# Kernel optimization log

Hardware: AMD Instinct MI355X
Metric: run time of the kernel (lower is better)

The kernel has to match this reference:

```python
import jax, jax.numpy as jnp
import numpy as np

DIM = 1024
HEADS = 16
HEAD_DIM = DIM // HEADS  # 64
EPS = 1e-5


def layer_norm(x, w, b):
    # LayerNorm over last dim (head_dim), matching nn.LayerNorm defaults
    mu = jnp.mean(x, axis=-1, keepdims=True)
    var = jnp.mean(jnp.square(x - mu), axis=-1, keepdims=True)
    return (x - mu) * jax.lax.rsqrt(var + EPS) * w + b


def apply_rotary_emb(x, freqs):
    # x: [B, S, H, D]; freqs: [S, D/2] angles. Interleaved (complex) rotary:
    # pairs (x[2i], x[2i+1]) rotated by angle freqs[:, i].
    x1 = x[..., 0::2]
    x2 = x[..., 1::2]
    cos = jnp.cos(freqs)[None, :, None, :]
    sin = jnp.sin(freqs)[None, :, None, :]
    r1 = x1 * cos - x2 * sin
    r2 = x1 * sin + x2 * cos
    return jnp.stack([r1, r2], axis=-1).reshape(x.shape)


def setup_inputs() -> dict:
    key = jax.random.key(0)
    ks = jax.random.split(key, 8)
    B, S = 2, 2048
    x = jax.random.normal(ks[0], (B, S, DIM), dtype=jnp.float32)
    freqs = jax.random.uniform(ks[1], (S, HEAD_DIM // 2), dtype=jnp.float32)
    sc = 1.0 / np.sqrt(DIM)
    w_qkv = jax.random.normal(ks[2], (DIM, 4 * DIM), dtype=jnp.float32) * sc
    w_out = jax.random.normal(ks[3], (DIM, DIM), dtype=jnp.float32) * sc
    qn_w = jnp.ones((HEAD_DIM,), jnp.float32)
    qn_b = jnp.zeros((HEAD_DIM,), jnp.float32)
    kn_w = jnp.ones((HEAD_DIM,), jnp.float32)
    kn_b = jnp.zeros((HEAD_DIM,), jnp.float32)
    return {"x": x, "freqs": freqs, "w_qkv": w_qkv, "w_out": w_out,
            "qn_w": qn_w, "qn_b": qn_b, "kn_w": kn_w, "kn_b": kn_b}


def reference(x, freqs, w_qkv, w_out, qn_w, qn_b, kn_w, kn_b):
    B, S, _ = x.shape
    qkv = x @ w_qkv  # [B, S, 4*DIM]
    q, k, v, gate = jnp.split(qkv, 4, axis=-1)
    q = q.reshape(B, S, HEADS, HEAD_DIM)
    k = k.reshape(B, S, HEADS, HEAD_DIM)
    v = v.reshape(B, S, HEADS, HEAD_DIM)
    q = layer_norm(q, qn_w, qn_b)
    k = layer_norm(k, kn_w, kn_b)
    q = apply_rotary_emb(q, freqs)
    k = apply_rotary_emb(k, freqs)
    # flash_attn_func: non-causal softmax attention, scale 1/sqrt(head_dim)
    scale = 1.0 / np.sqrt(HEAD_DIM)
    scores = jnp.einsum('bqhd,bkhd->bhqk', q, k) * scale
    probs = jax.nn.softmax(scores, axis=-1)
    o = jnp.einsum('bhqk,bkhd->bqhd', probs, v)
    o = o.reshape(B, S, DIM)
    o = o * jax.nn.sigmoid(gate)
    return o @ w_out
```

## Files before the change

kernel.cpp:

```cpp
#include <hip/hip_runtime.h>


typedef _Float16 f16;
typedef _Float16 f16x8 __attribute__((ext_vector_type(8)));
typedef _Float16 f16x4 __attribute__((ext_vector_type(4)));
typedef float    f32x4 __attribute__((ext_vector_type(4)));

#define MFMA16(a, b, c) __builtin_amdgcn_mfma_f32_16x16x32_f16((a), (b), (c), 0, 0, 0)

__device__ __forceinline__ void gload16(const void* g, void* l) {
  __builtin_amdgcn_global_load_lds(
      (const __attribute__((address_space(1))) void*)g,
      (__attribute__((address_space(3))) void*)l, 16, 0, 0);
}

__device__ __forceinline__ float exp2_fast(float x) {
#if __has_builtin(__builtin_amdgcn_exp2f)
  return __builtin_amdgcn_exp2f(x);
#else
  float r;
  asm("v_exp_f32 %0, %1" : "=v"(r) : "v"(x));
  return r;
#endif
}
__device__ __forceinline__ unsigned pkrtz(float a, float b) {
  typedef __fp16 hf16x2 __attribute__((ext_vector_type(2)));
  union { hf16x2 h; unsigned u; } c;
  c.h = __builtin_amdgcn_cvt_pkrtz(a, b);
  return c.u;
}

__global__ void rope_table_kernel(const float* __restrict__ freqs, float* __restrict__ tbl) {
  int i = blockIdx.x * 256 + threadIdx.x;
  if (i >= 2048 * 32) return;
  int s = i >> 5, j = i & 31;
  float f = freqs[i];
  tbl[s * 64 + j]      = cosf(f);
  tbl[s * 64 + 32 + j] = sinf(f);
}

__global__ void cast_f16_kernel(const float* __restrict__ in, f16* __restrict__ out, int n8) {
  int i = blockIdx.x * 256 + threadIdx.x;
  if (i >= n8) return;
  float4 a = ((const float4*)in)[2 * i];
  float4 b = ((const float4*)in)[2 * i + 1];
  f16x8 o;
  o[0] = (f16)a.x; o[1] = (f16)a.y; o[2] = (f16)a.z; o[3] = (f16)a.w;
  o[4] = (f16)b.x; o[5] = (f16)b.y; o[6] = (f16)b.z; o[7] = (f16)b.w;
  ((f16x8*)out)[i] = o;
}

__global__ void transpose_cast_kernel(const float* __restrict__ in, f16* __restrict__ out,
                                      int R, int C) {
  __shared__ float t[64][65];
  int c0 = blockIdx.x * 64, r0 = blockIdx.y * 64;
  int tx = threadIdx.x & 15, ty = threadIdx.x >> 4;
#pragma unroll
  for (int i = 0; i < 4; ++i) {
    float4 v = *(const float4*)&in[(size_t)(r0 + ty + 16 * i) * C + c0 + tx * 4];
    t[ty + 16 * i][tx * 4 + 0] = v.x;
    t[ty + 16 * i][tx * 4 + 1] = v.y;
    t[ty + 16 * i][tx * 4 + 2] = v.z;
    t[ty + 16 * i][tx * 4 + 3] = v.w;
  }
  __syncthreads();
#pragma unroll
  for (int i = 0; i < 4; ++i) {
    int n = c0 + ty + 16 * i;
    int k = r0 + tx * 4;
    f16x4 o;
    o[0] = (f16)t[tx * 4 + 0][ty + 16 * i];
    o[1] = (f16)t[tx * 4 + 1][ty + 16 * i];
    o[2] = (f16)t[tx * 4 + 2][ty + 16 * i];
    o[3] = (f16)t[tx * 4 + 3][ty + 16 * i];
    *(f16x4*)&out[(size_t)n * R + k] = o;
  }
}

__global__ void fill_debug_kernel(float* out, int n) {
  int i = blockIdx.x * 256 + threadIdx.x;
  if (i < n) out[i] = 12345.0f;
}

template <int EPI>
__global__ __launch_bounds__(256, 2) void gemm_f16(
    const f16* __restrict__ A, const f16* __restrict__ B,
    float* __restrict__ Cout, int M, int N, int K,
    float* __restrict__ q_f32, float* __restrict__ k_f32,
    float* __restrict__ gate_f32, f16* __restrict__ v_t) {
  __shared__ f16 sA[128 * 64], sB[128 * 64];
  const int tid = threadIdx.x, lane = tid & 63;
  const int wave = tid >> 6, wm = wave >> 1, wn = wave & 1;
  const int lg = lane >> 4, lr = lane & 15;
  const int n0 = blockIdx.x * 128, m0 = blockIdx.y * 128;

  f32x4 acc[4][4];
#pragma unroll
  for (int m = 0; m < 4; ++m)
#pragma unroll
    for (int n = 0; n < 4; ++n) acc[m][n] = (f32x4){0.f, 0.f, 0.f, 0.f};

  for (int k0 = 0; k0 < K; k0 += 64) {
#pragma unroll
    for (int r = 0; r < 4; ++r) {
      int off = (tid + r * 256) * 16;
      int row = off >> 7;
      int col = ((off & 127) ^ ((row & 7) << 4)) >> 1;
      gload16(A + (size_t)(m0 + row) * K + k0 + col, (char*)sA + off);
      gload16(B + (size_t)(n0 + row) * K + k0 + col, (char*)sB + off);
    }
    __syncthreads();
#pragma unroll
    for (int ks = 0; ks < 2; ++ks) {
      f16x8 bfr[4];
#pragma unroll
      for (int n = 0; n < 4; ++n) {
        int row = wn * 64 + n * 16 + lr;
        int boff = (row << 7) + (ks << 6) + (lg << 4);
        boff ^= (row & 7) << 4;
        bfr[n] = *(const f16x8*)((const char*)sB + boff);
      }
#pragma unroll
      for (int m = 0; m < 4; ++m) {
        int row = wm * 64 + m * 16 + lr;
        int aoff = (row << 7) + (ks << 6) + (lg << 4);
        aoff ^= (row & 7) << 4;
        f16x8 afr = *(const f16x8*)((const char*)sA + aoff);
#pragma unroll
        for (int n = 0; n < 4; ++n) acc[m][n] = MFMA16(afr, bfr[n], acc[m][n]);
      }
    }
    __syncthreads();
  }

  if (EPI == 0) {
#pragma unroll
    for (int m = 0; m < 4; ++m) {
      int row = m0 + wm * 64 + m * 16 + 4 * lg;
#pragma unroll
      for (int n = 0; n < 4; ++n) {
        int col = n0 + wn * 64 + n * 16 + lr;
#pragma unroll
        for (int r = 0; r < 4; ++r) Cout[(size_t)(row + r) * N + col] = acc[m][n][r];
      }
    }
  } else {
    int region = n0 >> 10;
#pragma unroll
    for (int m = 0; m < 4; ++m) {
      int row = m0 + wm * 64 + m * 16 + 4 * lg;
#pragma unroll
      for (int n = 0; n < 4; ++n) {
        int col = n0 + wn * 64 + n * 16 + lr;
        if (region == 0) {
#pragma unroll
          for (int r = 0; r < 4; ++r) q_f32[(size_t)(row + r) * 1024 + col] = acc[m][n][r];
        } else if (region == 1) {
#pragma unroll
          for (int r = 0; r < 4; ++r) k_f32[(size_t)(row + r) * 1024 + col - 1024] = acc[m][n][r];
        } else if (region == 3) {
#pragma unroll
          for (int r = 0; r < 4; ++r) gate_f32[(size_t)(row + r) * 1024 + col - 3072] = acc[m][n][r];
        } else {
          int c = col - 2048, hh = c >> 6, d = c & 63;
          int b = row >> 11, s = row & 2047;
          f16x4 pv;
          pv[0] = (f16)acc[m][n][0];
          pv[1] = (f16)acc[m][n][1];
          pv[2] = (f16)acc[m][n][2];
          pv[3] = (f16)acc[m][n][3];
          *(f16x4*)&v_t[(size_t)((b * 16 + hh) * 64 + d) * 2048 + s] = pv;
        }
      }
    }
  }
}

__global__ void norm_rope_kernel(const float* __restrict__ qf, const float* __restrict__ kf,
                                 const float* __restrict__ tbl,
                                 const float* __restrict__ qn_w, const float* __restrict__ qn_b,
                                 const float* __restrict__ kn_w, const float* __restrict__ kn_b,
                                 f16* __restrict__ q_h, f16* __restrict__ k_h) {
  int row = blockIdx.x;
  int s = row & 2047;
  int hh = threadIdx.x >> 4, sub = threadIdx.x & 15;
  int base = row * 1024 + hh * 64 + sub * 4;
  float c0 = tbl[s * 64 + sub * 2 + 0], c1 = tbl[s * 64 + sub * 2 + 1];
  float s0 = tbl[s * 64 + 32 + sub * 2 + 0], s1 = tbl[s * 64 + 32 + sub * 2 + 1];
#pragma unroll
  for (int which = 0; which < 2; ++which) {
    const float* src = which ? kf : qf;
    const float* wp = which ? kn_w : qn_w;
    const float* bp = which ? kn_b : qn_b;
    f16* dst = which ? k_h : q_h;
    float4 x = *(const float4*)&src[base];
    float sum = x.x + x.y + x.z + x.w;
    sum += __shfl_xor(sum, 1); sum += __shfl_xor(sum, 2);
    sum += __shfl_xor(sum, 4); sum += __shfl_xor(sum, 8);
    float mu = sum * (1.0f / 64.0f);
    float d0 = x.x - mu, d1 = x.y - mu, d2 = x.z - mu, d3 = x.w - mu;
    float sq = d0 * d0 + d1 * d1 + d2 * d2 + d3 * d3;
    sq += __shfl_xor(sq, 1); sq += __shfl_xor(sq, 2);
    sq += __shfl_xor(sq, 4); sq += __shfl_xor(sq, 8);
    float rstd = rsqrtf(sq * (1.0f / 64.0f) + 1e-5f);
    float4 w = *(const float4*)&wp[sub * 4];
    float4 bb = *(const float4*)&bp[sub * 4];
    float n0 = d0 * rstd * w.x + bb.x;
    float n1 = d1 * rstd * w.y + bb.y;
    float n2 = d2 * rstd * w.z + bb.z;
    float n3 = d3 * rstd * w.w + bb.w;
    float r0 = n0 * c0 - n1 * s0, r1 = n0 * s0 + n1 * c0;
    float r2 = n2 * c1 - n3 * s1, r3 = n2 * s1 + n3 * c1;
    f16x4 ov;
    ov[0] = (f16)r0; ov[1] = (f16)r1; ov[2] = (f16)r2; ov[3] = (f16)r3;
    *(f16x4*)&dst[base] = ov;
  }
}

__global__ __launch_bounds__(256, 2) void attn_kernel(const f16* __restrict__ q_h,
                                                      const f16* __restrict__ k_h,
                                                      const f16* __restrict__ v_t,
                                                      const float* __restrict__ gate_f32,
                                                      f16* __restrict__ a16) {
  __shared__ __align__(16) char smem[65536];
  const int tid = threadIdx.x, lane = tid & 63, wave = tid >> 6;
  const int lg = lane >> 4, lr = lane & 15;
  const int bh = blockIdx.x >> 4, qt = blockIdx.x & 15;
  const int b = bh >> 4, h = bh & 15;
  const int qrow0 = b * 2048 + qt * 128 + wave * 32;

  auto stage = [&](int kv0, int p) {
    char* kb = smem + p * 16384;
    char* vb = smem + 32768 + p * 16384;
#pragma unroll
    for (int r = 0; r < 4; ++r) {
      int off = (tid + r * 256) * 16;
      {
        int row = off >> 7;
        int col = ((off & 127) ^ ((row & 7) << 4)) >> 1;
        int g = ((row >> 5) << 5) + (((row >> 2) & 3) << 3) + (((row >> 4) & 1) << 2) + (row & 3);
        gload16(&k_h[(size_t)(b * 2048 + kv0 + g) * 1024 + h * 64 + col], kb + off);
      }
      {
        int d = off >> 8;
        int col = ((off & 255) ^ ((d & 15) << 4)) >> 1;
        gload16(&v_t[(size_t)(bh * 64 + d) * 2048 + kv0 + col], vb + off);
      }
    }
  };

  f16x8 qf[2][2];
#pragma unroll
  for (int n = 0; n < 2; ++n)
#pragma unroll
    for (int ks = 0; ks < 2; ++ks)
      qf[n][ks] = *(const f16x8*)&q_h[(size_t)(qrow0 + n * 16 + lr) * 1024 + h * 64 + ks * 32 + lg * 8];

  f16x8 ones;
#pragma unroll
  for (int j = 0; j < 8; ++j) ones[j] = (f16)1.0f;

  f32x4 accO[4][2];
#pragma unroll
  for (int m = 0; m < 4; ++m) {
    accO[m][0] = (f32x4){0.f, 0.f, 0.f, 0.f};
    accO[m][1] = (f32x4){0.f, 0.f, 0.f, 0.f};
  }
  f32x4 accL[2] = {(f32x4){0.f, 0.f, 0.f, 0.f}, (f32x4){0.f, 0.f, 0.f, 0.f}};
  float mrun[2] = {-1e30f, -1e30f};
  const float SCL2 = 0.125f * 1.44269504f;

  stage(0, 0);

  int cur = 0;
  for (int t = 0; t < 16; ++t, cur ^= 1) {
    __syncthreads();
    if (t < 15) stage((t + 1) * 128, cur ^ 1);

    const char* kb = smem + cur * 16384;
    const char* vb = smem + 32768 + cur * 16384;

    f32x4 st[8][2];
#pragma unroll
    for (int m = 0; m < 8; ++m) {
      st[m][0] = (f32x4){0.f, 0.f, 0.f, 0.f};
      st[m][1] = (f32x4){0.f, 0.f, 0.f, 0.f};
    }
    __builtin_amdgcn_s_setprio(1);
#pragma unroll
    for (int m = 0; m < 8; ++m)
#pragma unroll
      for (int ks = 0; ks < 2; ++ks) {
        int row = m * 16 + lr;
        int koff = (row << 7) + (ks << 6) + (lg << 4);
        koff ^= (row & 7) << 4;
        f16x8 a = *(const f16x8*)(kb + koff);
        st[m][0] = MFMA16(a, qf[0][ks], st[m][0]);
        st[m][1] = MFMA16(a, qf[1][ks], st[m][1]);
      }
    __builtin_amdgcn_s_setprio(0);

    uint2 pdw[2][8];
#pragma unroll
    for (int n = 0; n < 2; ++n) {
      float vm = st[0][n][0];
#pragma unroll
      for (int m = 0; m < 8; ++m)
#pragma unroll
        for (int r = 0; r < 4; ++r)
          if (m | r) vm = fmaxf(vm, st[m][n][r]);
      vm = fmaxf(vm, __shfl_xor(vm, 16));
      vm = fmaxf(vm, __shfl_xor(vm, 32));
      if (__any(vm > mrun[n])) {
        float mnew = fmaxf(mrun[n], vm);
        float fac = exp2_fast((mrun[n] - mnew) * SCL2);
        mrun[n] = mnew;
        accL[n] *= fac;
#pragma unroll
        for (int m = 0; m < 4; ++m) accO[m][n] *= fac;
      }
      float mc = mrun[n] * SCL2;
#pragma unroll
      for (int m = 0; m < 8; ++m) {
        float p0 = exp2_fast(st[m][n][0] * SCL2 - mc);
        float p1 = exp2_fast(st[m][n][1] * SCL2 - mc);
        float p2 = exp2_fast(st[m][n][2] * SCL2 - mc);
        float p3 = exp2_fast(st[m][n][3] * SCL2 - mc);
        pdw[n][m].x = pkrtz(p0, p1);
        pdw[n][m].y = pkrtz(p2, p3);
      }
    }

    f16x8 pb[2][4];
#pragma unroll
    for (int n = 0; n < 2; ++n)
#pragma unroll
      for (int ks = 0; ks < 4; ++ks) {
        union { uint4 u; f16x8 h; } c;
        c.u = make_uint4(pdw[n][2 * ks].x, pdw[n][2 * ks].y,
                         pdw[n][2 * ks + 1].x, pdw[n][2 * ks + 1].y);
        pb[n][ks] = c.h;
      }
    __builtin_amdgcn_s_setprio(1);
#pragma unroll
    for (int m = 0; m < 4; ++m)
#pragma unroll
      for (int ks = 0; ks < 4; ++ks) {
        int d = m * 16 + lr;
        int voff = (d << 8) + (ks << 6) + (lg << 4);
        voff ^= (d & 15) << 4;
        f16x8 av = *(const f16x8*)(vb + voff);
        accO[m][0] = MFMA16(av, pb[0][ks], accO[m][0]);
        accO[m][1] = MFMA16(av, pb[1][ks], accO[m][1]);
      }
#pragma unroll
    for (int ks = 0; ks < 4; ++ks) {
      accL[0] = MFMA16(ones, pb[0][ks], accL[0]);
      accL[1] = MFMA16(ones, pb[1][ks], accL[1]);
    }
    __builtin_amdgcn_s_setprio(0);
  }

#pragma unroll
  for (int n = 0; n < 2; ++n) {
    float rl = 1.0f / accL[n][0];
    int orow = qrow0 + n * 16 + lr;
#pragma unroll
    for (int m = 0; m < 4; ++m) {
      size_t idx = (size_t)orow * 1024 + h * 64 + m * 16 + lg * 4;
      float4 gv = *(const float4*)&gate_f32[idx];
      f16x4 ov;
      ov[0] = (f16)(accO[m][n][0] * rl / (1.f + __expf(-gv.x)));
      ov[1] = (f16)(accO[m][n][1] * rl / (1.f + __expf(-gv.y)));
      ov[2] = (f16)(accO[m][n][2] * rl / (1.f + __expf(-gv.z)));
      ov[3] = (f16)(accO[m][n][3] * rl / (1.f + __expf(-gv.w)));
      *(f16x4*)&a16[idx] = ov;
    }
  }
}

extern "C" void kernel_launch(void* const* d_in, const int* in_sizes, int n_in,
                              void* d_out, int out_size, void* d_ws, size_t ws_size,
                              hipStream_t stream) {
  const float* x      = (const float*)d_in[0];
  const float* freqs  = (const float*)d_in[1];
  const float* w_qkv  = (const float*)d_in[2];
  const float* w_out  = (const float*)d_in[3];
  const float* qn_w   = (const float*)d_in[4];
  const float* qn_b   = (const float*)d_in[5];
  const float* kn_w   = (const float*)d_in[6];
  const float* kn_b   = (const float*)d_in[7];
  float* out = (float*)d_out;
  char* ws = (char*)d_ws;
  const size_t MB = 1024 * 1024;
  float* q_f32    = (float*)(ws + 0);
  float* k_f32    = (float*)(ws + 16 * MB);
  float* gate_f32 = (float*)(ws + 32 * MB);
  f16*   v_t      = (f16*)(ws + 48 * MB);
  f16*   x16      = (f16*)(ws + 56 * MB);
  f16*   wq16     = (f16*)(ws + 64 * MB);
  f16*   wo16     = (f16*)(ws + 72 * MB);
  f16*   q_h      = (f16*)(ws + 74 * MB);
  f16*   k_h      = (f16*)(ws + 82 * MB);
  float* tbl      = (float*)(ws + 90 * MB);
  f16*   a16      = x16;

  if (ws_size < (size_t)91 * MB) {
    fill_debug_kernel<<<(out_size + 255) / 256, 256, 0, stream>>>(out, out_size);
    return;
  }

  rope_table_kernel<<<256, 256, 0, stream>>>(freqs, tbl);
  cast_f16_kernel<<<2048, 256, 0, stream>>>(x, x16, 524288);
  transpose_cast_kernel<<<dim3(64, 16), 256, 0, stream>>>(w_qkv, wq16, 1024, 4096);
  transpose_cast_kernel<<<dim3(16, 16), 256, 0, stream>>>(w_out, wo16, 1024, 1024);

  gemm_f16<1><<<dim3(32, 32), 256, 0, stream>>>(x16, wq16, nullptr, 4096, 4096, 1024,
                                                q_f32, k_f32, gate_f32, v_t);
  norm_rope_kernel<<<4096, 256, 0, stream>>>(q_f32, k_f32, tbl, qn_w, qn_b, kn_w, kn_b, q_h, k_h);
  attn_kernel<<<512, 256, 0, stream>>>(q_h, k_h, v_t, gate_f32, a16);
  gemm_f16<0><<<dim3(8, 32), 256, 0, stream>>>(a16, wo16, out, 4096, 1024, 1024,
                                               nullptr, nullptr, nullptr, nullptr);
}
```

Baseline: 155.5 us.

## Load K/V tiles directly from global into registers, dropping LDS staging

The attention kernel no longer stages K and V tiles through double-buffered shared memory with async global-to-LDS loads and block barriers. Each wave now reads its K and V fragments directly from global memory into registers every iteration. This removes the LDS traffic and __syncthreads, but all four waves in a block redundantly fetch the same K/V data, leaving it to cache. It also loses explicit prefetch overlap and raises register pressure.

```diff
diff --git a/kernel.cpp b/kernel.cpp
--- a/kernel.cpp
+++ b/kernel.cpp
@@ -222,32 +222,15 @@
                                                       const f16* __restrict__ v_t,
                                                       const float* __restrict__ gate_f32,
                                                       f16* __restrict__ a16) {
-  __shared__ __align__(16) char smem[65536];
   const int tid = threadIdx.x, lane = tid & 63, wave = tid >> 6;
   const int lg = lane >> 4, lr = lane & 15;
   const int bh = blockIdx.x >> 4, qt = blockIdx.x & 15;
   const int b = bh >> 4, h = bh & 15;
   const int qrow0 = b * 2048 + qt * 128 + wave * 32;
 
-  auto stage = [&](int kv0, int p) {
-    char* kb = smem + p * 16384;
-    char* vb = smem + 32768 + p * 16384;
-#pragma unroll
-    for (int r = 0; r < 4; ++r) {
-      int off = (tid + r * 256) * 16;
-      {
-        int row = off >> 7;
-        int col = ((off & 127) ^ ((row & 7) << 4)) >> 1;
-        int g = ((row >> 5) << 5) + (((row >> 2) & 3) << 3) + (((row >> 4) & 1) << 2) + (row & 3);
-        gload16(&k_h[(size_t)(b * 2048 + kv0 + g) * 1024 + h * 64 + col], kb + off);
-      }
-      {
-        int d = off >> 8;
-        int col = ((off & 255) ^ ((d & 15) << 4)) >> 1;
-        gload16(&v_t[(size_t)(bh * 64 + d) * 2048 + kv0 + col], vb + off);
-      }
-    }
-  };
+  const int sig_lane = ((lr >> 2) << 3) + (lr & 3);
+  const f16* kbase = k_h + ((size_t)(b * 2048 + sig_lane) << 10) + h * 64 + (lg << 3);
+  const f16* vbase = v_t + ((size_t)(bh * 64 + lr) << 11) + (lg << 3);
 
   f16x8 qf[2][2];
 #pragma unroll
@@ -270,15 +253,23 @@
   float mrun[2] = {-1e30f, -1e30f};
   const float SCL2 = 0.125f * 1.44269504f;
 
-  stage(0, 0);
-
-  int cur = 0;
-  for (int t = 0; t < 16; ++t, cur ^= 1) {
-    __syncthreads();
-    if (t < 15) stage((t + 1) * 128, cur ^ 1);
-
-    const char* kb = smem + cur * 16384;
-    const char* vb = smem + 32768 + cur * 16384;
+  for (int t = 0; t < 16; ++t) {
+    const int kv0 = t * 128;
+
+    f16x8 kf[8][2];
+#pragma unroll
+    for (int m = 0; m < 8; ++m) {
+      const f16* kp = kbase + ((size_t)(kv0 + ((m >> 1) << 5) + ((m & 1) << 2)) << 10);
+#pragma unroll
+      for (int ks = 0; ks < 2; ++ks) kf[m][ks] = *(const f16x8*)(kp + (ks << 5));
+    }
+    f16x8 vf[4][4];
+#pragma unroll
+    for (int m = 0; m < 4; ++m) {
+      const f16* vp = vbase + ((size_t)(m << 4) << 11) + kv0;
+#pragma unroll
+      for (int ks = 0; ks < 4; ++ks) vf[m][ks] = *(const f16x8*)(vp + (ks << 5));
+    }
 
     f32x4 st[8][2];
 #pragma unroll
@@ -291,12 +282,8 @@
     for (int m = 0; m < 8; ++m)
 #pragma unroll
       for (int ks = 0; ks < 2; ++ks) {
-        int row = m * 16 + lr;
-        int koff = (row << 7) + (ks << 6) + (lg << 4);
-        koff ^= (row & 7) << 4;
-        f16x8 a = *(const f16x8*)(kb + koff);
-        st[m][0] = MFMA16(a, qf[0][ks], st[m][0]);
-        st[m][1] = MFMA16(a, qf[1][ks], st[m][1]);
+        st[m][0] = MFMA16(kf[m][ks], qf[0][ks], st[m][0]);
+        st[m][1] = MFMA16(kf[m][ks], qf[1][ks], st[m][1]);
       }
     __builtin_amdgcn_s_setprio(0);
 
@@ -346,12 +333,8 @@
     for (int m = 0; m < 4; ++m)
 #pragma unroll
       for (int ks = 0; ks < 4; ++ks) {
-        int d = m * 16 + lr;
-        int voff = (d << 8) + (ks << 6) + (lg << 4);
-        voff ^= (d & 15) << 4;
-        f16x8 av = *(const f16x8*)(vb + voff);
-        accO[m][0] = MFMA16(av, pb[0][ks], accO[m][0]);
-        accO[m][1] = MFMA16(av, pb[1][ks], accO[m][1]);
+        accO[m][0] = MFMA16(vf[m][ks], pb[0][ks], accO[m][0]);
+        accO[m][1] = MFMA16(vf[m][ks], pb[1][ks], accO[m][1]);
       }
 #pragma unroll
     for (int ks = 0; ks < 4; ++ks) {
```

Measured after the change: 219.0 us. 1.41x slower.

## Double-buffer GEMM LDS tiles and add lazy softmax rescaling in attention

Applied to the files above, without the earlier changes.

The GEMM kernel now uses two LDS buffers, prefetching the next K tile while computing the current one, and drops the trailing barrier. In attention, the QK accumulation is restructured to chain MFMAs from zero, the row max uses a balanced tree, and the online softmax rescale is skipped unless the new max exceeds the running max by a threshold. This reduces stall and rescale overhead, at the cost of doubled GEMM LDS usage and unnormalized probabilities up to a bounded magnitude in fp16.

```diff
diff --git a/kernel.cpp b/kernel.cpp
--- a/kernel.cpp
+++ b/kernel.cpp
@@ -88,28 +88,35 @@
     float* __restrict__ Cout, int M, int N, int K,
     float* __restrict__ q_f32, float* __restrict__ k_f32,
     float* __restrict__ gate_f32, f16* __restrict__ v_t) {
-  __shared__ f16 sA[128 * 64], sB[128 * 64];
+  __shared__ f16 sA[2][128 * 64], sB[2][128 * 64];
   const int tid = threadIdx.x, lane = tid & 63;
   const int wave = tid >> 6, wm = wave >> 1, wn = wave & 1;
   const int lg = lane >> 4, lr = lane & 15;
   const int n0 = blockIdx.x * 128, m0 = blockIdx.y * 128;
 
-  f32x4 acc[4][4];
-#pragma unroll
-  for (int m = 0; m < 4; ++m)
-#pragma unroll
-    for (int n = 0; n < 4; ++n) acc[m][n] = (f32x4){0.f, 0.f, 0.f, 0.f};
-
-  for (int k0 = 0; k0 < K; k0 += 64) {
+  auto stg = [&](int k0, int p) {
 #pragma unroll
     for (int r = 0; r < 4; ++r) {
       int off = (tid + r * 256) * 16;
       int row = off >> 7;
       int col = ((off & 127) ^ ((row & 7) << 4)) >> 1;
-      gload16(A + (size_t)(m0 + row) * K + k0 + col, (char*)sA + off);
-      gload16(B + (size_t)(n0 + row) * K + k0 + col, (char*)sB + off);
-    }
+      gload16(A + (size_t)(m0 + row) * K + k0 + col, (char*)sA[p] + off);
+      gload16(B + (size_t)(n0 + row) * K + k0 + col, (char*)sB[p] + off);
+    }
+  };
+
+  f32x4 acc[4][4];
+#pragma unroll
+  for (int m = 0; m < 4; ++m)
+#pragma unroll
+    for (int n = 0; n < 4; ++n) acc[m][n] = (f32x4){0.f, 0.f, 0.f, 0.f};
+
+  stg(0, 0);
+  const int NT = K >> 6;
+  int cur = 0;
+  for (int t = 0; t < NT; ++t, cur ^= 1) {
     __syncthreads();
+    if (t + 1 < NT) stg((t + 1) << 6, cur ^ 1);
 #pragma unroll
     for (int ks = 0; ks < 2; ++ks) {
       f16x8 bfr[4];
@@ -118,19 +125,18 @@
         int row = wn * 64 + n * 16 + lr;
         int boff = (row << 7) + (ks << 6) + (lg << 4);
         boff ^= (row & 7) << 4;
-        bfr[n] = *(const f16x8*)((const char*)sB + boff);
+        bfr[n] = *(const f16x8*)((const char*)sB[cur] + boff);
       }
 #pragma unroll
       for (int m = 0; m < 4; ++m) {
         int row = wm * 64 + m * 16 + lr;
         int aoff = (row << 7) + (ks << 6) + (lg << 4);
         aoff ^= (row & 7) << 4;
-        f16x8 afr = *(const f16x8*)((const char*)sA + aoff);
+        f16x8 afr = *(const f16x8*)((const char*)sA[cur] + aoff);
 #pragma unroll
         for (int n = 0; n < 4; ++n) acc[m][n] = MFMA16(afr, bfr[n], acc[m][n]);
       }
     }
-    __syncthreads();
   }
 
   if (EPI == 0) {
@@ -269,6 +275,8 @@
   f32x4 accL[2] = {(f32x4){0.f, 0.f, 0.f, 0.f}, (f32x4){0.f, 0.f, 0.f, 0.f}};
   float mrun[2] = {-1e30f, -1e30f};
   const float SCL2 = 0.125f * 1.44269504f;
+  const float THRP = 44.36f;
+  const f32x4 fz = (f32x4){0.f, 0.f, 0.f, 0.f};
 
   stage(0, 0);
 
@@ -281,37 +289,34 @@
     const char* vb = smem + 32768 + cur * 16384;
 
     f32x4 st[8][2];
+    __builtin_amdgcn_s_setprio(1);
 #pragma unroll
     for (int m = 0; m < 8; ++m) {
-      st[m][0] = (f32x4){0.f, 0.f, 0.f, 0.f};
-      st[m][1] = (f32x4){0.f, 0.f, 0.f, 0.f};
-    }
-    __builtin_amdgcn_s_setprio(1);
-#pragma unroll
-    for (int m = 0; m < 8; ++m)
-#pragma unroll
-      for (int ks = 0; ks < 2; ++ks) {
-        int row = m * 16 + lr;
-        int koff = (row << 7) + (ks << 6) + (lg << 4);
-        koff ^= (row & 7) << 4;
-        f16x8 a = *(const f16x8*)(kb + koff);
-        st[m][0] = MFMA16(a, qf[0][ks], st[m][0]);
-        st[m][1] = MFMA16(a, qf[1][ks], st[m][1]);
-      }
+      int row = m * 16 + lr;
+      int koff0 = ((row << 7) + (lg << 4)) ^ ((row & 7) << 4);
+      int koff1 = ((row << 7) + 64 + (lg << 4)) ^ ((row & 7) << 4);
+      f16x8 a0 = *(const f16x8*)(kb + koff0);
+      f16x8 a1 = *(const f16x8*)(kb + koff1);
+      st[m][0] = MFMA16(a1, qf[0][1], MFMA16(a0, qf[0][0], fz));
+      st[m][1] = MFMA16(a1, qf[1][1], MFMA16(a0, qf[1][0], fz));
+    }
     __builtin_amdgcn_s_setprio(0);
 
     uint2 pdw[2][8];
 #pragma unroll
     for (int n = 0; n < 2; ++n) {
-      float vm = st[0][n][0];
-#pragma unroll
-      for (int m = 0; m < 8; ++m)
-#pragma unroll
-        for (int r = 0; r < 4; ++r)
-          if (m | r) vm = fmaxf(vm, st[m][n][r]);
+      float t03 = fmaxf(fmaxf(fmaxf(st[0][n][0], st[0][n][1]), fmaxf(st[0][n][2], st[0][n][3])),
+                        fmaxf(fmaxf(st[1][n][0], st[1][n][1]), fmaxf(st[1][n][2], st[1][n][3])));
+      float t47 = fmaxf(fmaxf(fmaxf(st[2][n][0], st[2][n][1]), fmaxf(st[2][n][2], st[2][n][3])),
+                        fmaxf(fmaxf(st[3][n][0], st[3][n][1]), fmaxf(st[3][n][2], st[3][n][3])));
+      float t8b = fmaxf(fmaxf(fmaxf(st[4][n][0], st[4][n][1]), fmaxf(st[4][n][2], st[4][n][3])),
+                        fmaxf(fmaxf(st[5][n][0], st[5][n][1]), fmaxf(st[5][n][2], st[5][n][3])));
+      float tcf = fmaxf(fmaxf(fmaxf(st[6][n][0], st[6][n][1]), fmaxf(st[6][n][2], st[6][n][3])),
+                        fmaxf(fmaxf(st[7][n][0], st[7][n][1]), fmaxf(st[7][n][2], st[7][n][3])));
+      float vm = fmaxf(fmaxf(t03, t47), fmaxf(t8b, tcf));
       vm = fmaxf(vm, __shfl_xor(vm, 16));
       vm = fmaxf(vm, __shfl_xor(vm, 32));
-      if (__any(vm > mrun[n])) {
+      if (__any(vm > mrun[n] + THRP)) {
         float mnew = fmaxf(mrun[n], vm);
         float fac = exp2_fast((mrun[n] - mnew) * SCL2);
         mrun[n] = mnew;
```

Result: faster. 150.6 us (-3.2%).
